# Performance work log

Hardware: AMD Instinct MI355X
Metric: run time of the kernel (lower is better)

## Reference

```python
import jax, jax.numpy as jnp
import numpy as np

NEG_INF = -1e30  # finite stand-in for -inf mask (exp underflows to 0 in fp32)
EPS = 1e-9       # kernel divides by (l + 1e-9)


def setup_inputs() -> dict:
    key = jax.random.key(0)
    kq, kk, kv = jax.random.split(key, 3)
    B, H, S, D = 1, 8, 2048, 64
    return {
        "Q": jax.random.normal(kq, (B, H, S, D), dtype=jnp.float32),
        "K": jax.random.normal(kk, (B, H, S, D), dtype=jnp.float32),
        "V": jax.random.normal(kv, (B, H, S, D), dtype=jnp.float32),
        "window_size": 128,
    }


def reference(Q, K, V, window_size):
    # Sliding-window local attention: for query s, keys t in [s-half, s+half] clipped to [0,S).
    B, H, S, D = Q.shape
    half = window_size // 2
    W = 2 * half + 1
    scale = 1.0 / np.sqrt(D).astype(np.float32)

    offs = jnp.arange(-half, half + 1)                 # [W]
    idx = jnp.arange(S)[:, None] + offs[None, :]       # [S, W]
    valid = (idx >= 0) & (idx < S)                     # [S, W]
    idxc = jnp.clip(idx, 0, S - 1)

    Kw = K[:, :, idxc]                                  # [B,H,S,W,D] banded gather
    Vw = V[:, :, idxc]                                  # [B,H,S,W,D]

    scores = jnp.einsum("bhsd,bhswd->bhsw", Q, Kw) * scale
    scores = jnp.where(valid[None, None], scores, NEG_INF)

    # online-softmax equivalent: stable softmax with kernel's epsilon in denominator
    m = jnp.max(scores, axis=-1, keepdims=True)         # [B,H,S,1]
    p = jnp.exp(scores - m)                             # [B,H,S,W]
    l = jnp.sum(p, axis=-1, keepdims=True)              # [B,H,S,1]
    out = jnp.einsum("bhsw,bhswd->bhsd", p, Vw) / (l + EPS)
    return out
```

## Files before the change

### kernel.cpp

```cpp
#include <hip/hip_runtime.h>
#include <math.h>

#define S_   2048
#define H_   8
#define D_   64
#define TQ   32
#define TK   160
#define HALF 64
#define PSD_W 36

__global__ __launch_bounds__(256, 2)
void swa_fwd(const float* __restrict__ Q, const float* __restrict__ K,
             const float* __restrict__ V, float* __restrict__ Out)
{
    __shared__ float4 Ks4[TK * 16];
    __shared__ float  psd[TK * PSD_W];

    const int t    = threadIdx.x;
    const int lane = t & 63;
    const int w8   = __builtin_amdgcn_readfirstlane((t >> 6) << 3);
    const int h    = blockIdx.y;
    const int q0   = blockIdx.x * TQ;
    const int k0   = q0 - HALF;

    const float* Kg = K + (size_t)h * S_ * D_;
    #pragma unroll
    for (int i = 0; i < (TK * 16) / 256; ++i) {
        const int idx = t + i * 256;
        const int j = idx >> 4, c = idx & 15;
        int gk = k0 + j;
        gk = gk < 0 ? 0 : (gk > S_ - 1 ? S_ - 1 : gk);
        const float4 v = *(const float4*)(Kg + gk * D_ + c * 4);
        Ks4[(j << 4) | (c ^ (j & 7))] = v;
    }
    {
        const float4 z = make_float4(0.f, 0.f, 0.f, 0.f);
        float4* p4 = (float4*)psd;
        for (int i = t; i < (TK * PSD_W) / 4; i += 256) p4[i] = z;
    }
    __syncthreads();

    const int jr0  = lane;
    const int jr1  = 64 + lane;
    const int jr2t = 128 + lane;
    const int jr2  = jr2t > TK - 1 ? TK - 1 : jr2t;
    const int sw0  = lane & 7;
    const int sw2  = jr2 & 7;

    float acc0[8], acc1[8], acc2[8];
    #pragma unroll
    for (int q = 0; q < 8; ++q) acc0[q] = acc1[q] = acc2[q] = 0.f;

    const float* Qw = Q + ((size_t)h * S_ + q0 + w8) * D_;

    #pragma unroll 2
    for (int c = 0; c < 16; ++c) {
        const float4 ka = Ks4[(jr0 << 4) | (c ^ sw0)];
        const float4 kb = Ks4[(jr1 << 4) | (c ^ sw0)];
        const float4 kc = Ks4[(jr2 << 4) | (c ^ sw2)];
        #pragma unroll
        for (int q = 0; q < 8; ++q) {
            const float4 qv = *(const float4*)(Qw + q * D_ + c * 4);
            acc0[q] = fmaf(ka.x, qv.x, acc0[q]);
            acc0[q] = fmaf(ka.y, qv.y, acc0[q]);
            acc0[q] = fmaf(ka.z, qv.z, acc0[q]);
            acc0[q] = fmaf(ka.w, qv.w, acc0[q]);
            acc1[q] = fmaf(kb.x, qv.x, acc1[q]);
            acc1[q] = fmaf(kb.y, qv.y, acc1[q]);
            acc1[q] = fmaf(kb.z, qv.z, acc1[q]);
            acc1[q] = fmaf(kb.w, qv.w, acc1[q]);
            acc2[q] = fmaf(kc.x, qv.x, acc2[q]);
            acc2[q] = fmaf(kc.y, qv.y, acc2[q]);
            acc2[q] = fmaf(kc.z, qv.z, acc2[q]);
            acc2[q] = fmaf(kc.w, qv.w, acc2[q]);
        }
    }

    const bool kv0 = (unsigned)(k0 + jr0)  < (unsigned)S_;
    const bool kv1 = (unsigned)(k0 + jr1)  < (unsigned)S_;
    const bool kv2 = (unsigned)(k0 + jr2t) < (unsigned)S_;
    const float scale = 0.125f;
    float l_[8];

    #pragma unroll
    for (int q = 0; q < 8; ++q) {
        const int sq   = w8 + q;
        const int off0 = jr0  - sq;
        const int off1 = jr1  - sq;
        const int off2 = jr2t - sq;
        const bool v0 = kv0 && ((unsigned)off0 <= 128u);
        const bool v1 = kv1 && ((unsigned)off1 <= 128u);
        const bool v2 = kv2 && ((unsigned)off2 <= 128u);
        const float x0 = v0 ? acc0[q] * scale : -1e30f;
        const float x1 = v1 ? acc1[q] * scale : -1e30f;
        const float x2 = v2 ? acc2[q] * scale : -1e30f;

        float m = fmaxf(x0, fmaxf(x1, x2));
        #pragma unroll
        for (int i = 1; i < 64; i <<= 1) m = fmaxf(m, __shfl_xor(m, i));

        const float p0 = __expf(x0 - m);
        const float p1 = __expf(x1 - m);
        const float p2 = __expf(x2 - m);

        float l = p0 + p1 + p2;
        #pragma unroll
        for (int i = 1; i < 64; i <<= 1) l += __shfl_xor(l, i);
        l_[q] = l;

        if ((unsigned)off0 <= 128u) psd[jr0  * PSD_W + sq] = p0;
        if ((unsigned)off1 <= 128u) psd[jr1  * PSD_W + sq] = p1;
        if ((unsigned)off2 <= 128u) psd[jr2t * PSD_W + sq] = p2;
    }

    float accO[8];
    #pragma unroll
    for (int q = 0; q < 8; ++q) accO[q] = 0.f;

    const float* Vg = V + (size_t)h * S_ * D_ + lane;

    #pragma unroll 8
    for (int jl = 0; jl < 136; ++jl) {
        const int jj = w8 + jl;
        int gk = k0 + jj;
        gk = gk < 0 ? 0 : (gk > S_ - 1 ? S_ - 1 : gk);
        const float vf = Vg[gk * D_];
        const float4 pa = *(const float4*)(psd + jj * PSD_W + w8);
        const float4 pb = *(const float4*)(psd + jj * PSD_W + w8 + 4);
        accO[0] = fmaf(pa.x, vf, accO[0]);
        accO[1] = fmaf(pa.y, vf, accO[1]);
        accO[2] = fmaf(pa.z, vf, accO[2]);
        accO[3] = fmaf(pa.w, vf, accO[3]);
        accO[4] = fmaf(pb.x, vf, accO[4]);
        accO[5] = fmaf(pb.y, vf, accO[5]);
        accO[6] = fmaf(pb.z, vf, accO[6]);
        accO[7] = fmaf(pb.w, vf, accO[7]);
    }

    float* Og = Out + ((size_t)h * S_ + q0 + w8) * D_ + lane;
    #pragma unroll
    for (int q = 0; q < 8; ++q)
        Og[q * D_] = accO[q] / (l_[q] + 1e-9f);
}

extern "C" void kernel_launch(void* const* d_in, const int* in_sizes, int n_in,
                              void* d_out, int out_size, void* d_ws, size_t ws_size,
                              hipStream_t stream)
{
    const float* Q = (const float*)d_in[0];
    const float* K = (const float*)d_in[1];
    const float* V = (const float*)d_in[2];
    float* Out = (float*)d_out;
    dim3 grid(S_ / TQ, H_);
    swa_fwd<<<grid, 256, 0, stream>>>(Q, K, V, Out);
}
```

Before: 87.00 us.

## Split query tile across 8 waves with per-wave packed probability buffer

```diff
diff --git a/kernel.cpp b/kernel.cpp
--- a/kernel.cpp
+++ b/kernel.cpp
@@ -1,65 +1,62 @@
 #include <hip/hip_runtime.h>
 #include <math.h>
 
-#define S_   2048
-#define H_   8
-#define D_   64
-#define TQ   32
-#define TK   160
-#define HALF 64
-#define PSD_W 36
+#define S_    2048
+#define H_    8
+#define D_    64
+#define TQ    32
+#define TK    160
+#define HALF  64
+#define PROWS 136
 
-__global__ __launch_bounds__(256, 2)
+__global__ __launch_bounds__(512, 4)
 void swa_fwd(const float* __restrict__ Q, const float* __restrict__ K,
              const float* __restrict__ V, float* __restrict__ Out)
 {
     __shared__ float4 Ks4[TK * 16];
-    __shared__ float  psd[TK * PSD_W];
+    __shared__ float4 psd2[8 * PROWS];
 
     const int t    = threadIdx.x;
     const int lane = t & 63;
-    const int w8   = __builtin_amdgcn_readfirstlane((t >> 6) << 3);
+    const int wv   = t >> 6;
+    const int w4   = wv << 2;
     const int h    = blockIdx.y;
     const int q0   = blockIdx.x * TQ;
     const int k0   = q0 - HALF;
 
     const float* Kg = K + (size_t)h * S_ * D_;
     #pragma unroll
-    for (int i = 0; i < (TK * 16) / 256; ++i) {
-        const int idx = t + i * 256;
+    for (int i = 0; i < (TK * 16) / 512; ++i) {
+        const int idx = t + i * 512;
         const int j = idx >> 4, c = idx & 15;
         int gk = k0 + j;
         gk = gk < 0 ? 0 : (gk > S_ - 1 ? S_ - 1 : gk);
-        const float4 v = *(const float4*)(Kg + gk * D_ + c * 4);
-        Ks4[(j << 4) | (c ^ (j & 7))] = v;
+        Ks4[(j << 4) | (c ^ (j & 7))] = *(const float4*)(Kg + gk * D_ + c * 4);
     }
     {
         const float4 z = make_float4(0.f, 0.f, 0.f, 0.f);
-        float4* p4 = (float4*)psd;
-        for (int i = t; i < (TK * PSD_W) / 4; i += 256) p4[i] = z;
+        for (int i = t; i < 8 * PROWS; i += 512) psd2[i] = z;
     }
     __syncthreads();
 
-    const int jr0  = lane;
-    const int jr1  = 64 + lane;
-    const int jr2t = 128 + lane;
+    const int jr0  = w4 + lane;
+    const int jr1  = w4 + 64 + lane;
+    const int jr2t = w4 + 128 + lane;
     const int jr2  = jr2t > TK - 1 ? TK - 1 : jr2t;
-    const int sw0  = lane & 7;
-    const int sw2  = jr2 & 7;
 
-    float acc0[8], acc1[8], acc2[8];
+    float acc0[4], acc1[4], acc2[4];
     #pragma unroll
-    for (int q = 0; q < 8; ++q) acc0[q] = acc1[q] = acc2[q] = 0.f;
+    for (int q = 0; q < 4; ++q) acc0[q] = acc1[q] = acc2[q] = 0.f;
 
-    const float* Qw = Q + ((size_t)h * S_ + q0 + w8) * D_;
+    const float* Qw = Q + ((size_t)h * S_ + q0 + w4) * D_;
 
     #pragma unroll 2
     for (int c = 0; c < 16; ++c) {
-        const float4 ka = Ks4[(jr0 << 4) | (c ^ sw0)];
-        const float4 kb = Ks4[(jr1 << 4) | (c ^ sw0)];
-        const float4 kc = Ks4[(jr2 << 4) | (c ^ sw2)];
+        const float4 ka = Ks4[(jr0 << 4) | (c ^ (jr0 & 7))];
+        const float4 kb = Ks4[(jr1 << 4) | (c ^ (jr1 & 7))];
+        const float4 kc = Ks4[(jr2 << 4) | (c ^ (jr2 & 7))];
         #pragma unroll
-        for (int q = 0; q < 8; ++q) {
+        for (int q = 0; q < 4; ++q) {
             const float4 qv = *(const float4*)(Qw + q * D_ + c * 4);
             acc0[q] = fmaf(ka.x, qv.x, acc0[q]);
             acc0[q] = fmaf(ka.y, qv.y, acc0[q]);
@@ -80,11 +77,11 @@
     const bool kv1 = (unsigned)(k0 + jr1)  < (unsigned)S_;
     const bool kv2 = (unsigned)(k0 + jr2t) < (unsigned)S_;
     const float scale = 0.125f;
-    float l_[8];
+    float l_[4];
 
     #pragma unroll
-    for (int q = 0; q < 8; ++q) {
-        const int sq   = w8 + q;
+    for (int q = 0; q < 4; ++q) {
+        const int sq   = w4 + q;
         const int off0 = jr0  - sq;
         const int off1 = jr1  - sq;
         const int off2 = jr2t - sq;
@@ -108,38 +105,34 @@
         for (int i = 1; i < 64; i <<= 1) l += __shfl_xor(l, i);
         l_[q] = l;
 
-        if ((unsigned)off0 <= 128u) psd[jr0  * PSD_W + sq] = p0;
-        if ((unsigned)off1 <= 128u) psd[jr1  * PSD_W + sq] = p1;
-        if ((unsigned)off2 <= 128u) psd[jr2t * PSD_W + sq] = p2;
+        float* pw = (float*)&psd2[wv * PROWS];
+        if ((unsigned)off0 <= 128u) pw[(jr0  - w4) * 4 + q] = p0;
+        if ((unsigned)off1 <= 128u) pw[(jr1  - w4) * 4 + q] = p1;
+        if ((unsigned)off2 <= 128u) pw[(jr2t - w4) * 4 + q] = p2;
     }
 
-    float accO[8];
+    float accO[4];
     #pragma unroll
-    for (int q = 0; q < 8; ++q) accO[q] = 0.f;
+    for (int q = 0; q < 4; ++q) accO[q] = 0.f;
 
     const float* Vg = V + (size_t)h * S_ * D_ + lane;
 
     #pragma unroll 8
-    for (int jl = 0; jl < 136; ++jl) {
-        const int jj = w8 + jl;
+    for (int jl = 0; jl < PROWS; ++jl) {
+        const int jj = w4 + jl;
         int gk = k0 + jj;
         gk = gk < 0 ? 0 : (gk > S_ - 1 ? S_ - 1 : gk);
         const float vf = Vg[gk * D_];
-        const float4 pa = *(const float4*)(psd + jj * PSD_W + w8);
-        const float4 pb = *(const float4*)(psd + jj * PSD_W + w8 + 4);
+        const float4 pa = psd2[wv * PROWS + jl];
         accO[0] = fmaf(pa.x, vf, accO[0]);
         accO[1] = fmaf(pa.y, vf, accO[1]);
         accO[2] = fmaf(pa.z, vf, accO[2]);
         accO[3] = fmaf(pa.w, vf, accO[3]);
-        accO[4] = fmaf(pb.x, vf, accO[4]);
-        accO[5] = fmaf(pb.y, vf, accO[5]);
-        accO[6] = fmaf(pb.z, vf, accO[6]);
-        accO[7] = fmaf(pb.w, vf, accO[7]);
     }
 
-    float* Og = Out + ((size_t)h * S_ + q0 + w8) * D_ + lane;
+    float* Og = Out + ((size_t)h * S_ + q0 + w4) * D_ + lane;
     #pragma unroll
-    for (int q = 0; q < 8; ++q)
+    for (int q = 0; q < 4; ++q)
         Og[q * D_] = accO[q] / (l_[q] + 1e-9f);
 }
 
@@ -152,5 +145,5 @@
     const float* V = (const float*)d_in[2];
     float* Out = (float*)d_out;
     dim3 grid(S_ / TQ, H_);
-    swa_fwd<<<grid, 256, 0, stream>>>(Q, K, V, Out);
+    swa_fwd<<<grid, 512, 0, stream>>>(Q, K, V, Out);
 }
```

Result: no change. 86.88 us (-0.1%).
